# Kernel tuning notes

Measured on AMD Instinct MI355X. Metric: run time of the kernel, lower is better.

The kernel has to match this reference:

```python
import jax, jax.numpy as jnp
import numpy as np

B = 64           # graphs
NPG = 2048       # nodes per graph
N = B * NPG      # total nodes
EPG = 32768      # edges per graph (avg degree 16)
E = B * EPG
D = 32           # in_features == out_features
RATIO = 0.5
K = int(NPG * RATIO)  # nodes kept per graph


def setup_inputs() -> dict:
    key = jax.random.key(0)
    ks = jax.random.split(key, 12)
    x = jax.random.normal(ks[0], (N, D), dtype=jnp.float32)
    gid = jnp.repeat(jnp.arange(B, dtype=jnp.int32), EPG)
    src = gid * NPG + jax.random.randint(ks[1], (E,), 0, NPG, dtype=jnp.int32)
    dst = gid * NPG + jax.random.randint(ks[2], (E,), 0, NPG, dtype=jnp.int32)
    edge_index = jnp.stack([src, dst])                      # [2, E]
    edge_attr = jax.random.uniform(ks[3], (E,), dtype=jnp.float32)
    batch = jnp.repeat(jnp.arange(B, dtype=jnp.int32), NPG)  # [N]
    s = 1.0 / np.sqrt(D)
    params = {}
    for i in range(3):
        params[f"W_root{i+1}"] = jax.random.normal(ks[4 + 2 * i], (D, D), dtype=jnp.float32) * s
        params[f"W_rel{i+1}"] = jax.random.normal(ks[5 + 2 * i], (D, D), dtype=jnp.float32) * s
        params[f"b{i+1}"] = jnp.zeros((D,), dtype=jnp.float32)
    return {"x": x, "edge_index": edge_index, "edge_attr": edge_attr, "batch": batch, **params}


def _graph_conv(x, src, dst, W_root, W_rel, b):
    # PyG GraphConv (aggr='add'): out_i = W_root x_i + W_rel * sum_{j->i} x_j + b
    agg = jax.ops.segment_sum(x[src], dst, num_segments=N)  # [N, D]
    return x @ W_root + agg @ W_rel + b


def reference(x, edge_index, edge_attr, batch,
              W_root1, W_rel1, b1, W_root2, W_rel2, b2, W_root3, W_rel3, b3):
    src, dst = edge_index[0], edge_index[1]
    x2 = _graph_conv(x, src, dst, W_root1, W_rel1, b1)  # [N, D]
    y2 = _graph_conv(x, src, dst, W_root2, W_rel2, b2)  # [N, D]
    # per-node attention score = <x2_i, y2_i> / sqrt(D)
    score = jnp.sum(x2 * y2, axis=-1) / jnp.sqrt(jnp.float32(D))  # [N]
    # topk per graph (equal-size graphs -> reshape + lax.top_k)
    _, top_idx = jax.lax.top_k(score.reshape(B, NPG), K)          # [B, K]
    perm = (top_idx + (jnp.arange(B, dtype=top_idx.dtype) * NPG)[:, None]).reshape(-1)  # [B*K]
    x3 = _graph_conv(x, src, dst, W_root3, W_rel3, b3)            # dropout_rate=0 -> identity
    # skip connection
    x5 = x[perm] + score[perm][:, None] * x3[perm]                # [B*K, D]
    new_batch = batch[perm]
    # filter_adj: relabel surviving nodes, mask (pad with -1 / 0) edges with a dropped endpoint
    new_idx = jnp.full((N,), -1, dtype=jnp.int32).at[perm].set(jnp.arange(perm.shape[0], dtype=jnp.int32))
    ns, nd = new_idx[src], new_idx[dst]
    valid = (ns >= 0) & (nd >= 0)
    new_edge_index = jnp.where(valid[None, :], jnp.stack([ns, nd]), -1)  # [2, E], -1 = dropped
    new_edge_attr = jnp.where(valid, edge_attr, 0.0)
    return (x5, new_edge_index, new_edge_attr, new_batch, perm, score[perm])
```

## Files before the change

kernel.cpp:

```cpp
#include <hip/hip_runtime.h>
#include <hip/hip_bf16.h>

#define NB   64
#define NPG  2048
#define NN   (NB*NPG)
#define EPG  32768
#define EE   (NB*EPG)
#define DD   32
#define KK   1024

typedef unsigned long long u64;
typedef unsigned int u32;

__global__ __launch_bounds__(1024) void hist_kernel(
    const int* __restrict__ dst, int* __restrict__ hist)
{
    __shared__ int cnt[NPG];
    int b = blockIdx.x;
    int t = threadIdx.x;
    int g = b & 63, s = b >> 6;
    for (int i = t; i < NPG; i += 1024) cnt[i] = 0;
    __syncthreads();
    const int ebase = g * EPG + s * 8192;
    const int nbase = g * NPG;
#pragma unroll
    for (int q = 0; q < 8; q++) {
        int e = ebase + q * 1024 + t;
        atomicAdd(&cnt[dst[e] - nbase], 1);
    }
    __syncthreads();
    int* hb = hist + (s * 64 + g) * NPG;
    for (int i = t; i < NPG; i += 1024) hb[i] = cnt[i];
}

__global__ __launch_bounds__(1024) void scan2_kernel(
    const int* __restrict__ hist,
    int* __restrict__ counts, int* __restrict__ offsets,
    int* __restrict__ cursors)
{
    __shared__ int tot[1024];
    int g = blockIdx.x;
    int t = threadIdx.x;
    int n0 = 2 * t, n1 = 2 * t + 1;
    int h0[4], h1[4];
#pragma unroll
    for (int s = 0; s < 4; s++) {
        h0[s] = hist[(s * 64 + g) * NPG + n0];
        h1[s] = hist[(s * 64 + g) * NPG + n1];
    }
    int c0 = h0[0] + h0[1] + h0[2] + h0[3];
    int c1 = h1[0] + h1[1] + h1[2] + h1[3];
    tot[t] = c0 + c1;
    __syncthreads();
    for (int o = 1; o < 1024; o <<= 1) {
        int v = tot[t];
        int u = (t >= o) ? tot[t - o] : 0;
        __syncthreads();
        tot[t] = v + u;
        __syncthreads();
    }
    int excl = (t == 0) ? 0 : tot[t - 1];
    int nbase = g * NPG;
    counts[nbase + n0] = c0;
    counts[nbase + n1] = c1;
    int off0 = g * EPG + excl;
    int off1 = off0 + c0;
    offsets[nbase + n0] = off0;
    offsets[nbase + n1] = off1;
    int a0 = off0, a1 = off1;
#pragma unroll
    for (int s = 0; s < 4; s++) {
        cursors[(s * 64 + g) * NPG + n0] = a0; a0 += h0[s];
        cursors[(s * 64 + g) * NPG + n1] = a1; a1 += h1[s];
    }
}

__global__ __launch_bounds__(1024) void scatter_kernel(
    const int* __restrict__ src, const int* __restrict__ dst,
    const int* __restrict__ cursors, int* __restrict__ edge_ids)
{
    __shared__ int cur[NPG];
    int b = blockIdx.x;
    int t = threadIdx.x;
    int g = b & 63, s = b >> 6;
    const int* cb = cursors + (s * 64 + g) * NPG;
    for (int i = t; i < NPG; i += 1024) cur[i] = cb[i];
    __syncthreads();
    const int ebase = g * EPG + s * 8192;
    const int nbase = g * NPG;
#pragma unroll
    for (int q = 0; q < 8; q++) {
        int e = ebase + q * 1024 + t;
        int pos = atomicAdd(&cur[dst[e] - nbase], 1);
        edge_ids[pos] = src[e];
    }
}

__global__ __launch_bounds__(256) void agg_kernel(
    const float* __restrict__ x,
    const int* __restrict__ counts, const int* __restrict__ offsets,
    const int* __restrict__ edge_ids,
    float* __restrict__ agg)
{
    const float SCALE  = 4194304.0f;
    const float ISCALE = 2.38418579101562e-07f;
    int b = blockIdx.x;
    int c = (b & 7) * 512 + (b >> 3);
    int tid = c * 256 + threadIdx.x;
    int node = tid >> 3;
    int ch = (tid & 7) * 4;
    int deg  = counts[node];
    int base = offsets[node];
    int ax = 0, ay = 0, az = 0, aw = 0;
    for (int k = 0; k < deg; k++) {
        int s = edge_ids[base + k];
        float4 v = *(const float4*)(x + (long long)s * DD + ch);
        ax += __float2int_rn(v.x * SCALE);
        ay += __float2int_rn(v.y * SCALE);
        az += __float2int_rn(v.z * SCALE);
        aw += __float2int_rn(v.w * SCALE);
    }
    float4 r;
    r.x = (float)ax * ISCALE;
    r.y = (float)ay * ISCALE;
    r.z = (float)az * ISCALE;
    r.w = (float)aw * ISCALE;
    *(float4*)(agg + (long long)node * DD + ch) = r;
}

__global__ __launch_bounds__(256) void score_kernel(
    const float* __restrict__ x, const float* __restrict__ agg,
    const float* __restrict__ Wr1, const float* __restrict__ Wl1, const float* __restrict__ b1,
    const float* __restrict__ Wr2, const float* __restrict__ Wl2, const float* __restrict__ b2,
    float* __restrict__ score)
{
    __shared__ float4 sWr1[DD*DD/4], sWl1[DD*DD/4], sWr2[DD*DD/4], sWl2[DD*DD/4];
    __shared__ float sb1[DD], sb2[DD];
    __shared__ float2 part[128];
    {
        int t = threadIdx.x;
        sWr1[t] = ((const float4*)Wr1)[t];
        sWl1[t] = ((const float4*)Wl1)[t];
        sWr2[t] = ((const float4*)Wr2)[t];
        sWl2[t] = ((const float4*)Wl2)[t];
        if (t < DD) { sb1[t] = b1[t]; sb2[t] = b2[t]; }
    }
    __syncthreads();

    int lane = threadIdx.x & 127;
    int half = threadIdx.x >> 7;
    int i0 = blockIdx.x * 128 + lane;
    int i1 = i0 + NN/2;

    float xv0[DD], av0[DD], xv1[DD], av1[DD];
    {
        const float4* xp0 = (const float4*)(x + (long long)i0 * DD);
        const float4* ap0 = (const float4*)(agg + (long long)i0 * DD);
        const float4* xp1 = (const float4*)(x + (long long)i1 * DD);
        const float4* ap1 = (const float4*)(agg + (long long)i1 * DD);
#pragma unroll
        for (int q = 0; q < 8; q++) {
            float4 v0 = xp0[q]; xv0[4*q]=v0.x; xv0[4*q+1]=v0.y; xv0[4*q+2]=v0.z; xv0[4*q+3]=v0.w;
            float4 w0 = ap0[q]; av0[4*q]=w0.x; av0[4*q+1]=w0.y; av0[4*q+2]=w0.z; av0[4*q+3]=w0.w;
            float4 v1 = xp1[q]; xv1[4*q]=v1.x; xv1[4*q+1]=v1.y; xv1[4*q+2]=v1.z; xv1[4*q+3]=v1.w;
            float4 w1 = ap1[q]; av1[4*q]=w1.x; av1[4*q+1]=w1.y; av1[4*q+2]=w1.z; av1[4*q+3]=w1.w;
        }
    }

    float sc0 = 0.f, sc1 = 0.f;
    int dbase = half * 4;
    for (int dd = 0; dd < 4; dd++) {
        int d0 = dbase + dd;
        float a0[4], q0[4], a1[4], q1[4];
#pragma unroll
        for (int j = 0; j < 4; j++) {
            a0[j] = sb1[4*d0+j]; q0[j] = sb2[4*d0+j];
            a1[j] = sb1[4*d0+j]; q1[j] = sb2[4*d0+j];
        }
#pragma unroll
        for (int k = 0; k < DD; k++) {
            float4 wr1 = sWr1[k*8 + d0];
            float4 wl1 = sWl1[k*8 + d0];
            float4 wr2 = sWr2[k*8 + d0];
            float4 wl2 = sWl2[k*8 + d0];
            const float* r1 = &wr1.x; const float* l1 = &wl1.x;
            const float* r2 = &wr2.x; const float* l2 = &wl2.x;
            float xk0 = xv0[k], ak0 = av0[k];
            float xk1 = xv1[k], ak1 = av1[k];
#pragma unroll
            for (int j = 0; j < 4; j++) {
                a0[j] += xk0 * r1[j];
                a0[j] += ak0 * l1[j];
                q0[j] += xk0 * r2[j];
                q0[j] += ak0 * l2[j];
                a1[j] += xk1 * r1[j];
                a1[j] += ak1 * l1[j];
                q1[j] += xk1 * r2[j];
                q1[j] += ak1 * l2[j];
            }
        }
#pragma unroll
        for (int j = 0; j < 4; j++) { sc0 += a0[j] * q0[j]; sc1 += a1[j] * q1[j]; }
    }

    if (half) { part[lane].x = sc0; part[lane].y = sc1; }
    __syncthreads();
    if (!half) {
        float2 p = part[lane];
        score[i0] = (sc0 + p.x) * 0.17677669529663687f;
        score[i1] = (sc1 + p.y) * 0.17677669529663687f;
    }
}

__global__ __launch_bounds__(1024) void topk_kernel(
    const float* __restrict__ score,
    int* __restrict__ perm_int, int* __restrict__ new_idx,
    float* __restrict__ out_perm,
    float* __restrict__ out_batch,
    float* __restrict__ out_score)
{
    __shared__ u64 keys[NPG];
    int b = blockIdx.x;
    int t = threadIdx.x;
    const float* s = score + (long long)b * NPG;

    for (int j = t; j < NPG; j += 1024) {
        u32 u = __float_as_uint(s[j]);
        u32 h = (u & 0x80000000u) ? u : ~(u | 0x80000000u);
        keys[j] = ((u64)h << 32) | (u32)j;
    }

    for (int k = 2; k <= NPG; k <<= 1) {
        for (int j = k >> 1; j > 0; j >>= 1) {
            __syncthreads();
            int i = ((t & ~(j - 1)) << 1) | (t & (j - 1));
            int l = i | j;
            u64 a = keys[i], c = keys[l];
            bool up = ((i & k) == 0);
            if ((a > c) == up) { keys[i] = c; keys[l] = a; }
        }
    }
    __syncthreads();

    u64 kk = keys[t];
    int idx = (int)(u32)(kk & 0xFFFFFFFFu);
    int g = b * NPG + idx;
    int o = b * KK + t;
    perm_int[o] = g;
    new_idx[g] = o;
    out_perm[o]  = (float)g;
    out_batch[o] = (float)b;
    out_score[o] = s[idx];

    u64 kd = keys[t + KK];
    int idxd = (int)(u32)(kd & 0xFFFFFFFFu);
    new_idx[b * NPG + idxd] = -1;
}

__global__ __launch_bounds__(256) void x5_kernel(
    const float* __restrict__ x, const float* __restrict__ agg,
    const float* __restrict__ Wr3, const float* __restrict__ Wl3, const float* __restrict__ b3,
    const int* __restrict__ perm_int, const float* __restrict__ score,
    float* __restrict__ out_x5)
{
    __shared__ float4 sWr[DD*DD/4], sWl[DD*DD/4];
    __shared__ float sb[DD];
    {
        int t = threadIdx.x;
        sWr[t] = ((const float4*)Wr3)[t];
        sWl[t] = ((const float4*)Wl3)[t];
        if (t < DD) sb[t] = b3[t];
    }
    __syncthreads();

    int lane = threadIdx.x & 127;
    int half = threadIdx.x >> 7;
    int i = blockIdx.x * 128 + lane;
    int g = perm_int[i];
    float sc = score[g];

    float xv[DD], av[DD];
    {
        const float4* xp = (const float4*)(x + (long long)g * DD);
        const float4* ap = (const float4*)(agg + (long long)g * DD);
#pragma unroll
        for (int q = 0; q < 8; q++) {
            float4 v = xp[q]; xv[4*q]=v.x; xv[4*q+1]=v.y; xv[4*q+2]=v.z; xv[4*q+3]=v.w;
            float4 w = ap[q]; av[4*q]=w.x; av[4*q+1]=w.y; av[4*q+2]=w.z; av[4*q+3]=w.w;
        }
    }

    float* outp = out_x5 + (long long)i * DD;
    int dbase = half * 4;
    for (int dd = 0; dd < 4; dd++) {
        int d0 = dbase + dd;
        float a[4];
#pragma unroll
        for (int j = 0; j < 4; j++) a[j] = sb[4*d0+j];
#pragma unroll
        for (int k = 0; k < DD; k++) {
            float xk = xv[k], ak = av[k];
            float4 wr = sWr[k*8 + d0];
            float4 wl = sWl[k*8 + d0];
            const float* rp = &wr.x; const float* lp = &wl.x;
#pragma unroll
            for (int j = 0; j < 4; j++) {
                a[j] += xk * rp[j];
                a[j] += ak * lp[j];
            }
        }
#pragma unroll
        for (int j = 0; j < 4; j++) outp[4*d0+j] = xv[4*d0+j] + sc * a[j];
    }
}

__global__ __launch_bounds__(256) void edge_kernel(
    const int* __restrict__ src, const int* __restrict__ dst,
    const float* __restrict__ edge_attr,
    const int* __restrict__ new_idx,
    float* __restrict__ out_ei,
    float* __restrict__ out_attr)
{
    int e = (blockIdx.x * 256 + threadIdx.x) * 4;
    if (e >= EE) return;
    int4 s4 = *(const int4*)(src + e);
    int4 d4 = *(const int4*)(dst + e);
    float4 at = *(const float4*)(edge_attr + e);

    int ns[4] = { new_idx[s4.x], new_idx[s4.y], new_idx[s4.z], new_idx[s4.w] };
    int nd[4] = { new_idx[d4.x], new_idx[d4.y], new_idx[d4.z], new_idx[d4.w] };
    float av[4] = { at.x, at.y, at.z, at.w };

    float4 os, od, oa;
    float* osp = &os.x; float* odp = &od.x; float* oap = &oa.x;
#pragma unroll
    for (int j = 0; j < 4; j++) {
        bool valid = (ns[j] >= 0) && (nd[j] >= 0);
        osp[j] = (float)(valid ? ns[j] : -1);
        odp[j] = (float)(valid ? nd[j] : -1);
        oap[j] = valid ? av[j] : 0.f;
    }
    *(float4*)(out_ei + e)      = os;
    *(float4*)(out_ei + EE + e) = od;
    *(float4*)(out_attr + e)    = oa;
}

extern "C" void kernel_launch(void* const* d_in, const int* in_sizes, int n_in,
                              void* d_out, int out_size, void* d_ws, size_t ws_size,
                              hipStream_t stream)
{
    const float* x     = (const float*)d_in[0];
    const int*   src   = (const int*)d_in[1];
    const int*   dst   = ((const int*)d_in[1]) + EE;
    const float* eattr = (const float*)d_in[2];
    const float* Wr1 = (const float*)d_in[4];
    const float* Wl1 = (const float*)d_in[5];
    const float* b1  = (const float*)d_in[6];
    const float* Wr2 = (const float*)d_in[7];
    const float* Wl2 = (const float*)d_in[8];
    const float* b2  = (const float*)d_in[9];
    const float* Wr3 = (const float*)d_in[10];
    const float* Wl3 = (const float*)d_in[11];
    const float* b3  = (const float*)d_in[12];

    char* ws = (char*)d_ws;
    int*   counts   = (int*)  (ws + 0);
    int*   offsets  = (int*)  (ws + (size_t)NN*4);
    float* score    = (float*)(ws + (size_t)NN*8);
    int*   perm_int = (int*)  (ws + (size_t)NN*12);
    int*   new_idx  = (int*)  (ws + (size_t)NN*12 + (size_t)NB*KK*4);
    int*   hist     = (int*)  (ws + (size_t)NN*16 + (size_t)NB*KK*4);
    int*   cursors  = (int*)  (ws + (size_t)NN*32 + (size_t)NB*KK*4);

    float* out = (float*)d_out;
    float* out_x5    = out;
    float* out_ei    = out + (size_t)NB*KK*DD;
    float* out_attr  = out_ei + (size_t)2*EE;
    float* out_batch = out_attr + (size_t)EE;
    float* out_perm  = out_batch + (size_t)NB*KK;
    float* out_score = out_perm + (size_t)NB*KK;

    float* agg      = out_ei;
    int*   edge_ids = (int*)out_attr;

    hist_kernel   <<<256, 1024, 0, stream>>>(dst, hist);
    scan2_kernel  <<<NB, 1024, 0, stream>>>(hist, counts, offsets, cursors);
    scatter_kernel<<<256, 1024, 0, stream>>>(src, dst, cursors, edge_ids);

    agg_kernel  <<<(NN*8)/256, 256, 0, stream>>>(x, counts, offsets, edge_ids, agg);

    score_kernel<<<NN/256, 256, 0, stream>>>(x, agg, Wr1, Wl1, b1, Wr2, Wl2, b2, score);

    topk_kernel<<<NB, 1024, 0, stream>>>(score, perm_int, new_idx,
                                         out_perm, out_batch, out_score);

    x5_kernel<<<(NB*KK)/128, 256, 0, stream>>>(x, agg, Wr3, Wl3, b3,
                                               perm_int, score, out_x5);

    edge_kernel<<<(EE/4)/256, 256, 0, stream>>>(src, dst, eattr, new_idx, out_ei, out_attr);
}
```

Before: 220.4 us.

## Replace CSR build and gather aggregation with bucketed scatter and LDS atomic accumulation

The histogram, scan and cursor-scatter kernels that built a per-node CSR are replaced by one kernel. It bins each graph's edges into four destination-quarter buckets using wave ballots, packing the src and dst locals into one int. A new aggregation kernel gives each block one graph quarter, accumulates fixed-point sums with LDS integer atomics in a swizzled layout, then writes agg out. This cuts kernel launches and avoids the global CSR passes. In exchange it relies on a fixed bucket capacity (QCAP) that could overflow for skewed degree distributions, and it adds heavy LDS atomic contention.

Result: faster. 206.6 us (-6.3%).

```diff
diff --git a/kernel.cpp b/kernel.cpp
--- a/kernel.cpp
+++ b/kernel.cpp
@@ -9,123 +9,112 @@
 #define DD   32
 #define KK   1024
 
+#define QCAP 2560
+
 typedef unsigned long long u64;
 typedef unsigned int u32;
 
-__global__ __launch_bounds__(1024) void hist_kernel(
-    const int* __restrict__ dst, int* __restrict__ hist)
-{
-    __shared__ int cnt[NPG];
-    int b = blockIdx.x;
-    int t = threadIdx.x;
+__global__ __launch_bounds__(1024) void qscatter_kernel(
+    const int* __restrict__ src, const int* __restrict__ dst,
+    int* __restrict__ qcnt, int* __restrict__ packed)
+{
+    __shared__ int wcnt[16][4];
+    __shared__ int wbase[16][4];
+    int b = blockIdx.x, t = threadIdx.x;
     int g = b & 63, s = b >> 6;
-    for (int i = t; i < NPG; i += 1024) cnt[i] = 0;
-    __syncthreads();
+    int w = t >> 6, lane = t & 63;
     const int ebase = g * EPG + s * 8192;
     const int nbase = g * NPG;
-#pragma unroll
-    for (int q = 0; q < 8; q++) {
-        int e = ebase + q * 1024 + t;
-        atomicAdd(&cnt[dst[e] - nbase], 1);
-    }
-    __syncthreads();
-    int* hb = hist + (s * 64 + g) * NPG;
-    for (int i = t; i < NPG; i += 1024) hb[i] = cnt[i];
-}
-
-__global__ __launch_bounds__(1024) void scan2_kernel(
-    const int* __restrict__ hist,
-    int* __restrict__ counts, int* __restrict__ offsets,
-    int* __restrict__ cursors)
-{
-    __shared__ int tot[1024];
-    int g = blockIdx.x;
-    int t = threadIdx.x;
-    int n0 = 2 * t, n1 = 2 * t + 1;
-    int h0[4], h1[4];
-#pragma unroll
+    u64 ltmask = (1ull << lane) - 1ull;
+
+    int pk[8], qv[8], pos[8];
+    int wq0 = 0, wq1 = 0, wq2 = 0, wq3 = 0;
+#pragma unroll
+    for (int r = 0; r < 8; r++) {
+        int e  = ebase + r * 1024 + t;
+        int sl = src[e] - nbase;
+        int dl = dst[e] - nbase;
+        int q  = dl >> 9;
+        pk[r] = (sl << 9) | (dl & 511);
+        qv[r] = q;
+        u64 b0 = __ballot(q == 0);
+        u64 b1 = __ballot(q == 1);
+        u64 b2 = __ballot(q == 2);
+        u64 b3 = __ballot(q == 3);
+        int rk = (q == 0) ? wq0 + __popcll(b0 & ltmask)
+               : (q == 1) ? wq1 + __popcll(b1 & ltmask)
+               : (q == 2) ? wq2 + __popcll(b2 & ltmask)
+                          : wq3 + __popcll(b3 & ltmask);
+        pos[r] = rk;
+        wq0 += __popcll(b0); wq1 += __popcll(b1);
+        wq2 += __popcll(b2); wq3 += __popcll(b3);
+    }
+    if (lane == 0) {
+        wcnt[w][0] = wq0; wcnt[w][1] = wq1;
+        wcnt[w][2] = wq2; wcnt[w][3] = wq3;
+    }
+    __syncthreads();
+    if (t < 4) {
+        int run = 0;
+        for (int ww = 0; ww < 16; ww++) { wbase[ww][t] = run; run += wcnt[ww][t]; }
+        qcnt[((s * 64 + g) << 2) + t] = run;
+    }
+    __syncthreads();
+    const int rbase = (s * 64 + g) << 2;
+#pragma unroll
+    for (int r = 0; r < 8; r++) {
+        int q = qv[r];
+        packed[(size_t)(rbase + q) * QCAP + wbase[w][q] + pos[r]] = pk[r];
+    }
+}
+
+__global__ __launch_bounds__(1024) void agg2_kernel(
+    const float* __restrict__ x,
+    const int* __restrict__ qcnt, const int* __restrict__ packed,
+    float* __restrict__ agg)
+{
+    __shared__ int acc[512 * DD];
+    int b = blockIdx.x, t = threadIdx.x;
+    int g = b & 63, q = b >> 6;
+    for (int i = t; i < 512 * DD; i += 1024) acc[i] = 0;
+    __syncthreads();
+
+    const float SCALE = 4194304.0f;
+    const float* xg = x + (size_t)g * NPG * DD;
+    int sub   = t & 3;
+    int ei0   = t >> 2;
+    int dbase = sub << 3;
+
     for (int s = 0; s < 4; s++) {
-        h0[s] = hist[(s * 64 + g) * NPG + n0];
-        h1[s] = hist[(s * 64 + g) * NPG + n1];
-    }
-    int c0 = h0[0] + h0[1] + h0[2] + h0[3];
-    int c1 = h1[0] + h1[1] + h1[2] + h1[3];
-    tot[t] = c0 + c1;
-    __syncthreads();
-    for (int o = 1; o < 1024; o <<= 1) {
-        int v = tot[t];
-        int u = (t >= o) ? tot[t - o] : 0;
-        __syncthreads();
-        tot[t] = v + u;
-        __syncthreads();
-    }
-    int excl = (t == 0) ? 0 : tot[t - 1];
-    int nbase = g * NPG;
-    counts[nbase + n0] = c0;
-    counts[nbase + n1] = c1;
-    int off0 = g * EPG + excl;
-    int off1 = off0 + c0;
-    offsets[nbase + n0] = off0;
-    offsets[nbase + n1] = off1;
-    int a0 = off0, a1 = off1;
-#pragma unroll
-    for (int s = 0; s < 4; s++) {
-        cursors[(s * 64 + g) * NPG + n0] = a0; a0 += h0[s];
-        cursors[(s * 64 + g) * NPG + n1] = a1; a1 += h1[s];
-    }
-}
-
-__global__ __launch_bounds__(1024) void scatter_kernel(
-    const int* __restrict__ src, const int* __restrict__ dst,
-    const int* __restrict__ cursors, int* __restrict__ edge_ids)
-{
-    __shared__ int cur[NPG];
-    int b = blockIdx.x;
-    int t = threadIdx.x;
-    int g = b & 63, s = b >> 6;
-    const int* cb = cursors + (s * 64 + g) * NPG;
-    for (int i = t; i < NPG; i += 1024) cur[i] = cb[i];
-    __syncthreads();
-    const int ebase = g * EPG + s * 8192;
-    const int nbase = g * NPG;
-#pragma unroll
-    for (int q = 0; q < 8; q++) {
-        int e = ebase + q * 1024 + t;
-        int pos = atomicAdd(&cur[dst[e] - nbase], 1);
-        edge_ids[pos] = src[e];
-    }
-}
-
-__global__ __launch_bounds__(256) void agg_kernel(
-    const float* __restrict__ x,
-    const int* __restrict__ counts, const int* __restrict__ offsets,
-    const int* __restrict__ edge_ids,
-    float* __restrict__ agg)
-{
-    const float SCALE  = 4194304.0f;
+        int n = qcnt[((s * 64 + g) << 2) + q];
+        const int* pb = packed + (size_t)(((s * 64 + g) << 2) + q) * QCAP;
+        for (int i = ei0; i < n; i += 256) {
+            int pkv = pb[i];
+            int dl  = pkv & 511;
+            int sl  = pkv >> 9;
+            const float4* xp = (const float4*)(xg + sl * DD + dbase);
+            float4 v0 = xp[0];
+            float4 v1 = xp[1];
+            int* ar = acc + (dl << 5);
+            int  m  = dl & 31;
+            atomicAdd(ar + ((dbase + 0) ^ m), __float2int_rn(v0.x * SCALE));
+            atomicAdd(ar + ((dbase + 1) ^ m), __float2int_rn(v0.y * SCALE));
+            atomicAdd(ar + ((dbase + 2) ^ m), __float2int_rn(v0.z * SCALE));
+            atomicAdd(ar + ((dbase + 3) ^ m), __float2int_rn(v0.w * SCALE));
+            atomicAdd(ar + ((dbase + 4) ^ m), __float2int_rn(v1.x * SCALE));
+            atomicAdd(ar + ((dbase + 5) ^ m), __float2int_rn(v1.y * SCALE));
+            atomicAdd(ar + ((dbase + 6) ^ m), __float2int_rn(v1.z * SCALE));
+            atomicAdd(ar + ((dbase + 7) ^ m), __float2int_rn(v1.w * SCALE));
+        }
+    }
+    __syncthreads();
+
     const float ISCALE = 2.38418579101562e-07f;
-    int b = blockIdx.x;
-    int c = (b & 7) * 512 + (b >> 3);
-    int tid = c * 256 + threadIdx.x;
-    int node = tid >> 3;
-    int ch = (tid & 7) * 4;
-    int deg  = counts[node];
-    int base = offsets[node];
-    int ax = 0, ay = 0, az = 0, aw = 0;
-    for (int k = 0; k < deg; k++) {
-        int s = edge_ids[base + k];
-        float4 v = *(const float4*)(x + (long long)s * DD + ch);
-        ax += __float2int_rn(v.x * SCALE);
-        ay += __float2int_rn(v.y * SCALE);
-        az += __float2int_rn(v.z * SCALE);
-        aw += __float2int_rn(v.w * SCALE);
-    }
-    float4 r;
-    r.x = (float)ax * ISCALE;
-    r.y = (float)ay * ISCALE;
-    r.z = (float)az * ISCALE;
-    r.w = (float)aw * ISCALE;
-    *(float4*)(agg + (long long)node * DD + ch) = r;
+    float* ao = agg + ((size_t)g * NPG + (size_t)q * 512) * DD;
+    for (int i = t; i < 512 * DD; i += 1024) {
+        int row = i >> 5, d = i & 31;
+        ao[i] = (float)acc[(row << 5) | (d ^ (row & 31))] * ISCALE;
+    }
 }
 
 __global__ __launch_bounds__(256) void score_kernel(
@@ -364,13 +353,11 @@
     const float* b3  = (const float*)d_in[12];
 
     char* ws = (char*)d_ws;
-    int*   counts   = (int*)  (ws + 0);
-    int*   offsets  = (int*)  (ws + (size_t)NN*4);
-    float* score    = (float*)(ws + (size_t)NN*8);
-    int*   perm_int = (int*)  (ws + (size_t)NN*12);
-    int*   new_idx  = (int*)  (ws + (size_t)NN*12 + (size_t)NB*KK*4);
-    int*   hist     = (int*)  (ws + (size_t)NN*16 + (size_t)NB*KK*4);
-    int*   cursors  = (int*)  (ws + (size_t)NN*32 + (size_t)NB*KK*4);
+    float* score    = (float*)(ws + 0);
+    int*   perm_int = (int*)  (ws + (size_t)NN*4);
+    int*   new_idx  = (int*)  (ws + (size_t)NN*4 + (size_t)NB*KK*4);
+    int*   qcnt     = (int*)  (ws + (size_t)NN*8 + (size_t)NB*KK*4);
+    int*   packed   = (int*)  (ws + (size_t)NN*8 + (size_t)NB*KK*4 + 4096);
 
     float* out = (float*)d_out;
     float* out_x5    = out;
@@ -380,14 +367,11 @@
     float* out_perm  = out_batch + (size_t)NB*KK;
     float* out_score = out_perm + (size_t)NB*KK;
 
-    float* agg      = out_ei;
-    int*   edge_ids = (int*)out_attr;
-
-    hist_kernel   <<<256, 1024, 0, stream>>>(dst, hist);
-    scan2_kernel  <<<NB, 1024, 0, stream>>>(hist, counts, offsets, cursors);
-    scatter_kernel<<<256, 1024, 0, stream>>>(src, dst, cursors, edge_ids);
-
-    agg_kernel  <<<(NN*8)/256, 256, 0, stream>>>(x, counts, offsets, edge_ids, agg);
+    float* agg = out_ei;
+
+    qscatter_kernel<<<256, 1024, 0, stream>>>(src, dst, qcnt, packed);
+
+    agg2_kernel<<<256, 1024, 0, stream>>>(x, qcnt, packed, agg);
 
     score_kernel<<<NN/256, 256, 0, stream>>>(x, agg, Wr1, Wl1, b1, Wr2, Wl2, b2, score);
 
```
